# Performance work log

Hardware: AMD Instinct MI355X
Metric: run time of the kernel (lower is better)

Reference implementation:

```python
import jax, jax.numpy as jnp
import numpy as np

N = 100000   # nodes
E = 1600000  # edges
NF = 8       # node features
H = 128      # hid_channel


def _gcn(x, ei, W, b):
    """PyG GCNConv: add self-loops, sym-normalize, x@W then scatter-add, +bias."""
    n = x.shape[0]
    loop = jnp.arange(n)
    s = jnp.concatenate([ei[0], loop])
    d = jnp.concatenate([ei[1], loop])
    deg = jax.ops.segment_sum(jnp.ones_like(s, jnp.float32), d, num_segments=n)
    dinv = jnp.where(deg > 0, jax.lax.rsqrt(deg), 0.0)
    norm = dinv[s] * dinv[d]                       # [E+n]
    xw = x @ W                                     # [n, out]
    out = jax.ops.segment_sum(xw[s] * norm[:, None], d, num_segments=n)
    return out + b


def _dag_pool(x, ei, k):
    """DAGPool(k): contiguous-k mean clustering; unpool restores saved (x, ei)."""
    n = x.shape[0]
    nc = -(-n // k)
    cid = jnp.arange(n) // k
    cnt = jax.ops.segment_sum(jnp.ones((n,), jnp.float32), cid, num_segments=nc)
    xp = jax.ops.segment_sum(x, cid, num_segments=nc) / cnt[:, None]
    return xp, ei // k, (x, ei)


def setup_inputs() -> dict:
    key = jax.random.key(0)
    ks = jax.random.split(key, 24)

    def w(k, i, o):
        return jax.random.normal(k, (i, o), jnp.float32) / np.sqrt(i).astype(np.float32)

    d = {
        "x": jax.random.normal(ks[0], (N, NF), jnp.float32),
        "edge_index": jax.random.randint(ks[1], (E, 2), 0, N, dtype=jnp.int64),
        "c1W": w(ks[2], NF, H),          "c1b": jnp.zeros((H,), jnp.float32),
        "c2W": w(ks[3], H + NF, H),      "c2b": jnp.zeros((H,), jnp.float32),
        "c3W": w(ks[4], H + NF, H),      "c3b": jnp.zeros((H,), jnp.float32),
        "c4W": w(ks[5], H, H),           "c4b": jnp.zeros((H,), jnp.float32),
        "c5W": w(ks[6], H, H),           "c5b": jnp.zeros((H,), jnp.float32),
        "f1W": w(ks[7], 2 * H + NF, H),  "f1b": jnp.zeros((H,), jnp.float32),
        "f2W": w(ks[8], 2 * H, H),       "f2b": jnp.zeros((H,), jnp.float32),
        "f3W": w(ks[9], 2 * H, H),       "f3b": jnp.zeros((H,), jnp.float32),
        "f4W": w(ks[10], H + NF, H),     "f4b": jnp.zeros((H,), jnp.float32),
        "f5W": w(ks[11], H + NF, 1),     "f5b": jnp.zeros((1,), jnp.float32),
    }
    return d


def reference(x, edge_index, c1W, c1b, c2W, c2b, c3W, c3b, c4W, c4b, c5W, c5b,
              f1W, f1b, f2W, f2b, f3W, f3b, f4W, f4b, f5W, f5b):
    ei = edge_index.T  # [2, E]
    x_in = x
    h = jax.nn.relu(_gcn(x, ei, c1W, c1b))
    h = jnp.concatenate([h, x_in], axis=-1)
    h = jax.nn.relu(_gcn(h, ei, c2W, c2b))
    h = jnp.concatenate([x_in, h], axis=-1)            # [N, NF+H]

    xp1, ei1, un1 = _dag_pool(h, ei, 5)
    t = jax.nn.relu(_gcn(xp1, ei1, c3W, c3b))
    t = jax.nn.relu(jnp.concatenate([xp1, t], -1) @ f1W + f1b)
    xp2, ei2, un2 = _dag_pool(t, ei1, 3)
    t = jax.nn.relu(_gcn(xp2, ei2, c4W, c4b))
    t = jax.nn.relu(jnp.concatenate([xp2, t], -1) @ f2W + f2b)
    xp3, ei3, un3 = _dag_pool(t, ei2, 3)
    t = jax.nn.relu(_gcn(xp3, ei3, c5W, c5b))
    t = jax.nn.relu(jnp.concatenate([xp3, t], -1) @ f3W + f3b)
    # unpool chain discards pooled features and restores pre-pool1 state
    xr, _ = un1

    h = jax.nn.relu(xr @ f4W + f4b)
    out = jax.nn.sigmoid(jnp.concatenate([x_in, h], -1) @ f5W + f5b)
    return out.ravel()  # [N], binary (num_classes==2 -> 1 logit)
```

## Files before the change

kernel.cpp:

```cpp
#include <hip/hip_runtime.h>
#include <hip/hip_bf16.h>
#include <math.h>


#define NBUK 256

typedef __attribute__((ext_vector_type(8))) short short8;
typedef __attribute__((ext_vector_type(4))) float f32x4;

__device__ __forceinline__ unsigned short f32_to_bf16_rne(float f) {
    unsigned u = __float_as_uint(f);
    return (unsigned short)((u + 0x7fffu + ((u >> 16) & 1u)) >> 16);
}

__global__ __launch_bounds__(512) void bucket_kernel(
    const int* __restrict__ ei, int* __restrict__ bcnt_pad,
    int2* __restrict__ bucket, int E, int N, int cap) {
    constexpr int EPB = 4096;
    __shared__ int lcnt[NBUK];
    __shared__ int lcur[NBUK];
    int e0 = blockIdx.x * EPB;
    int e1 = min(e0 + EPB, E);
    if (threadIdx.x < NBUK) lcnt[threadIdx.x] = 0;
    __syncthreads();
    for (int e = e0 + threadIdx.x; e < e1; e += 512) {
        int2 v = ((const int2*)ei)[e];
        if ((unsigned)v.y < (unsigned)N) {
            int b = (int)(((unsigned long long)(unsigned)v.y * NBUK) / (unsigned)N);
            atomicAdd(&lcnt[b], 1);
        }
    }
    __syncthreads();
    if (threadIdx.x < NBUK)
        lcur[threadIdx.x] = atomicAdd(&bcnt_pad[threadIdx.x * 16], lcnt[threadIdx.x]);
    __syncthreads();
    for (int e = e0 + threadIdx.x; e < e1; e += 512) {
        int2 v = ((const int2*)ei)[e];
        if ((unsigned)v.y < (unsigned)N) {
            int b = (int)(((unsigned long long)(unsigned)v.y * NBUK) / (unsigned)N);
            int pos = atomicAdd(&lcur[b], 1);
            if (pos < cap) {
                int s = ((unsigned)v.x < (unsigned)N) ? v.x : 0;
                bucket[(size_t)b * cap + pos] = make_int2(s, v.y);
            }
        }
    }
}

__global__ __launch_bounds__(1024) void csr_kernel(
    const int2* __restrict__ bucket, const int* __restrict__ bcnt_pad,
    const float* __restrict__ x,
    int* __restrict__ cnt, int* __restrict__ rowstart, int* __restrict__ col,
    float* __restrict__ dinv, float* __restrict__ xs,
    unsigned short* __restrict__ Abf2, int N, int cap) {
    __shared__ int lcnt[1024];
    __shared__ int lscan[1024];
    int b = blockIdx.x;
    int lo = (int)(((long long)b * N + NBUK - 1) / NBUK);
    int hi = (int)(((long long)(b + 1) * N + NBUK - 1) / NBUK);
    int range = hi - lo;
    lcnt[threadIdx.x] = 0;
    __syncthreads();
    int n = min(bcnt_pad[b * 16], cap);
    const int2* bk = bucket + (size_t)b * cap;
    for (int i = threadIdx.x; i < n; i += 1024)
        atomicAdd(&lcnt[bk[i].y - lo], 1);
    __syncthreads();
    int myc = lcnt[threadIdx.x];
    if ((int)threadIdx.x < range) cnt[lo + threadIdx.x] = myc;
    lscan[threadIdx.x] = myc;
    __syncthreads();
    for (int off = 1; off < 1024; off <<= 1) {
        int y = (threadIdx.x >= off) ? lscan[threadIdx.x - off] : 0;
        __syncthreads();
        lscan[threadIdx.x] += y;
        __syncthreads();
    }
    int colbase = b * cap;
    int excl = lscan[threadIdx.x] - myc;
    if ((int)threadIdx.x < range) rowstart[lo + threadIdx.x] = colbase + excl;
    lcnt[threadIdx.x] = excl;
    __syncthreads();
    for (int i = threadIdx.x; i < n; i += 1024) {
        int2 v = bk[i];
        int pos = atomicAdd(&lcnt[v.y - lo], 1);
        col[(size_t)colbase + pos] = v.x;
    }
    if ((int)threadIdx.x < range) {
        int v = lo + threadIdx.x;
        float dv = rsqrtf((float)(myc + 1));
        dinv[v] = dv;
        const float4* x4 = (const float4*)x;
        float4 a = x4[v * 2], c = x4[v * 2 + 1];
        float4* o = (float4*)xs;
        o[v * 2]     = make_float4(a.x * dv, a.y * dv, a.z * dv, a.w * dv);
        o[v * 2 + 1] = make_float4(c.x * dv, c.y * dv, c.z * dv, c.w * dv);
        unsigned short u[8] = {f32_to_bf16_rne(a.x), f32_to_bf16_rne(a.y),
                               f32_to_bf16_rne(a.z), f32_to_bf16_rne(a.w),
                               f32_to_bf16_rne(c.x), f32_to_bf16_rne(c.y),
                               f32_to_bf16_rne(c.z), f32_to_bf16_rne(c.w)};
        ulonglong2 pk;
        pk.x = (unsigned long long)u[0] | ((unsigned long long)u[1] << 16)
             | ((unsigned long long)u[2] << 32) | ((unsigned long long)u[3] << 48);
        pk.y = (unsigned long long)u[4] | ((unsigned long long)u[5] << 16)
             | ((unsigned long long)u[6] << 32) | ((unsigned long long)u[7] << 48);
        *(ulonglong2*)&Abf2[(size_t)v * 160] = pk;
        ulonglong2 z; z.x = 0ull; z.y = 0ull;
        *(ulonglong2*)&Abf2[(size_t)v * 160 + 136] = z;
        *(ulonglong2*)&Abf2[(size_t)v * 160 + 144] = z;
        *(ulonglong2*)&Abf2[(size_t)v * 160 + 152] = z;
    }
}

__global__ __launch_bounds__(256) void agg8_kernel(const float* __restrict__ xs,
                                                   const int* __restrict__ rowstart,
                                                   const int* __restrict__ cnt,
                                                   const int* __restrict__ col,
                                                   const float* __restrict__ dinv,
                                                   float* __restrict__ aggx,
                                                   unsigned short* __restrict__ Abf,
                                                   int n) {
    int v = blockIdx.x * 256 + threadIdx.x;
    if (v >= n) return;
    const float4* r4 = (const float4*)xs;
    float4 a = make_float4(0, 0, 0, 0), b = make_float4(0, 0, 0, 0);
    int start = rowstart[v];
    int end = start + cnt[v];
    for (int j = start; j < end; j++) {
        int s = col[j];
        float4 p = r4[(size_t)s * 2], q = r4[(size_t)s * 2 + 1];
        a.x += p.x; a.y += p.y; a.z += p.z; a.w += p.w;
        b.x += q.x; b.y += q.y; b.z += q.z; b.w += q.w;
    }
    float4 p = r4[(size_t)v * 2], q = r4[(size_t)v * 2 + 1];
    a.x += p.x; a.y += p.y; a.z += p.z; a.w += p.w;
    b.x += q.x; b.y += q.y; b.z += q.z; b.w += q.w;
    float dv = dinv[v];
    a = make_float4(a.x * dv, a.y * dv, a.z * dv, a.w * dv);
    b = make_float4(b.x * dv, b.y * dv, b.z * dv, b.w * dv);
    float4* o = (float4*)aggx;
    o[(size_t)v * 2]     = a;
    o[(size_t)v * 2 + 1] = b;
    unsigned short u[8] = {f32_to_bf16_rne(a.x), f32_to_bf16_rne(a.y),
                           f32_to_bf16_rne(a.z), f32_to_bf16_rne(a.w),
                           f32_to_bf16_rne(b.x), f32_to_bf16_rne(b.y),
                           f32_to_bf16_rne(b.z), f32_to_bf16_rne(b.w)};
    ulonglong2 pk;
    pk.x = (unsigned long long)u[0] | ((unsigned long long)u[1] << 16)
         | ((unsigned long long)u[2] << 32) | ((unsigned long long)u[3] << 48);
    pk.y = (unsigned long long)u[4] | ((unsigned long long)u[5] << 16)
         | ((unsigned long long)u[6] << 32) | ((unsigned long long)u[7] << 48);
    *(ulonglong2*)&Abf[(size_t)v * 160 + 128] = pk;
    ulonglong2 z; z.x = 0ull; z.y = 0ull;
    *(ulonglong2*)&Abf[(size_t)v * 160 + 136] = z;
    *(ulonglong2*)&Abf[(size_t)v * 160 + 144] = z;
    *(ulonglong2*)&Abf[(size_t)v * 160 + 152] = z;
}

__global__ __launch_bounds__(256) void agg128_kernel(const unsigned* __restrict__ rows,
                                                     const int* __restrict__ rowstart,
                                                     const int* __restrict__ cnt,
                                                     const int* __restrict__ col,
                                                     const float* __restrict__ dinv,
                                                     unsigned short* __restrict__ Abf,
                                                     int n) {
    int v = blockIdx.x * 4 + (threadIdx.x >> 6);
    int lane = threadIdx.x & 63;
    if (v >= n) return;
    float ax = 0.f, ay = 0.f;
    int start = rowstart[v];
    int end = start + cnt[v];
    for (int base = start; base < end; base += 64) {
        int m = end - base; if (m > 64) m = 64;
        int si = (lane < m) ? col[base + lane] : 0;
        int t = 0;
        for (; t + 4 <= m; t += 4) {
            int s0 = __shfl(si, t),     s1 = __shfl(si, t + 1);
            int s2 = __shfl(si, t + 2), s3 = __shfl(si, t + 3);
            unsigned u0 = rows[(size_t)s0 * 64 + lane];
            unsigned u1 = rows[(size_t)s1 * 64 + lane];
            unsigned u2 = rows[(size_t)s2 * 64 + lane];
            unsigned u3 = rows[(size_t)s3 * 64 + lane];
            ax += (__uint_as_float(u0 << 16) + __uint_as_float(u1 << 16))
                + (__uint_as_float(u2 << 16) + __uint_as_float(u3 << 16));
            ay += (__uint_as_float(u0 & 0xffff0000u) + __uint_as_float(u1 & 0xffff0000u))
                + (__uint_as_float(u2 & 0xffff0000u) + __uint_as_float(u3 & 0xffff0000u));
        }
        for (; t < m; t++) {
            int s = __shfl(si, t);
            unsigned u = rows[(size_t)s * 64 + lane];
            ax += __uint_as_float(u << 16);
            ay += __uint_as_float(u & 0xffff0000u);
        }
    }
    unsigned us = rows[(size_t)v * 64 + lane];
    ax += __uint_as_float(us << 16);
    ay += __uint_as_float(us & 0xffff0000u);
    float dv = dinv[v];
    unsigned pk = (unsigned)f32_to_bf16_rne(ax * dv)
                | ((unsigned)f32_to_bf16_rne(ay * dv) << 16);
    ((unsigned*)Abf)[(size_t)v * 80 + lane] = pk;
}

__global__ __launch_bounds__(256) void gemm8_kernel(
    const float* __restrict__ A1, const float* __restrict__ W,
    const float* __restrict__ bias, const float* __restrict__ dinv,
    unsigned short* __restrict__ out, int n) {
    constexpr int K = 8, KP = 12, NPB = 32;
    __shared__ float lds[NPB * KP];
    int node0 = blockIdx.x * NPB;
    for (int idx = threadIdx.x; idx < NPB * K; idx += 256) {
        int r = idx / K, k = idx - r * K;
        int node = node0 + r;
        lds[r * KP + k] = (node < n) ? A1[(size_t)node * K + k] : 0.f;
    }
    __syncthreads();
    int f8 = threadIdx.x & 15, ng = threadIdx.x >> 4;
    int fbase = f8 * 8;
    float acc[2][8];
#pragma unroll
    for (int r = 0; r < 2; r++)
#pragma unroll
        for (int j = 0; j < 8; j++) acc[r][j] = 0.f;
    for (int k = 0; k < K; k += 4) {
        float4 wlo[4], whi[4];
#pragma unroll
        for (int kk = 0; kk < 4; kk++) {
            wlo[kk] = *(const float4*)&W[(size_t)(k + kk) * 128 + fbase];
            whi[kk] = *(const float4*)&W[(size_t)(k + kk) * 128 + fbase + 4];
        }
#pragma unroll
        for (int r = 0; r < 2; r++) {
            float4 a = *(const float4*)&lds[(2 * ng + r) * KP + k];
            float av[4] = {a.x, a.y, a.z, a.w};
#pragma unroll
            for (int kk = 0; kk < 4; kk++) {
                acc[r][0] += av[kk] * wlo[kk].x; acc[r][1] += av[kk] * wlo[kk].y;
                acc[r][2] += av[kk] * wlo[kk].z; acc[r][3] += av[kk] * wlo[kk].w;
                acc[r][4] += av[kk] * whi[kk].x; acc[r][5] += av[kk] * whi[kk].y;
                acc[r][6] += av[kk] * whi[kk].z; acc[r][7] += av[kk] * whi[kk].w;
            }
        }
    }
    float4 blo = *(const float4*)&bias[fbase];
    float4 bhi = *(const float4*)&bias[fbase + 4];
    float bv[8] = {blo.x, blo.y, blo.z, blo.w, bhi.x, bhi.y, bhi.z, bhi.w};
#pragma unroll
    for (int r = 0; r < 2; r++) {
        int node = node0 + 2 * ng + r;
        if (node < n) {
            float dv = dinv[node];
            unsigned short u[8];
#pragma unroll
            for (int j = 0; j < 8; j++)
                u[j] = f32_to_bf16_rne(fmaxf(acc[r][j] + bv[j], 0.f) * dv);
            ulonglong2 pk;
            pk.x = (unsigned long long)u[0] | ((unsigned long long)u[1] << 16)
                 | ((unsigned long long)u[2] << 32) | ((unsigned long long)u[3] << 48);
            pk.y = (unsigned long long)u[4] | ((unsigned long long)u[5] << 16)
                 | ((unsigned long long)u[6] << 32) | ((unsigned long long)u[7] << 48);
            *(ulonglong2*)&out[(size_t)node * 128 + fbase] = pk;
        }
    }
}

__global__ __launch_bounds__(256) void pack_w_kernel(const float* __restrict__ W,
                                                     unsigned short* __restrict__ wp, int K) {
    int t = blockIdx.x * 256 + threadIdx.x;
    if (t >= 20480) return;
    int i = t & 7, l = (t >> 3) & 63, fc = (t >> 9) & 7, ks = t >> 12;
    int k = ks * 32 + (l >> 4) * 8 + i;
    int c = (l & 15) + 16 * fc;
    float v = (k < K) ? W[(size_t)k * 128 + c] : 0.f;
    wp[t] = f32_to_bf16_rne(v);
}

template <int MODE>
__global__ __launch_bounds__(256) void mfma_gemm(
    const unsigned short* __restrict__ A, const unsigned short* __restrict__ wp,
    const float* __restrict__ bias, const float* __restrict__ x,
    const float* __restrict__ f5W, const float* __restrict__ f5b,
    void* __restrict__ outv, int n) {
    __shared__ float ldsx[64];
    int node0 = blockIdx.x * 64;
    if constexpr (MODE == 2) {
        if (threadIdx.x < 64) {
            int rc = min(node0 + (int)threadIdx.x, n - 1);
            float s = 0.f;
#pragma unroll
            for (int k = 0; k < 8; k++) s += x[(size_t)rc * 8 + k] * f5W[k];
            ldsx[threadIdx.x] = s;
        }
        __syncthreads();
    }
    int wave = threadIdx.x >> 6, lane = threadIdx.x & 63;
    int g = lane >> 4, r = lane & 15;
    int row0 = node0 + wave * 16;
    int arow = min(row0 + r, n - 1);

    short8 a[5];
#pragma unroll
    for (int ks = 0; ks < 5; ks++)
        a[ks] = *(const short8*)&A[(size_t)arow * 160 + ks * 32 + g * 8];

    f32x4 acc[8] = {};
#pragma unroll
    for (int ks = 0; ks < 5; ks++) {
#pragma unroll
        for (int fc = 0; fc < 8; fc++) {
            short8 w = *(const short8*)&wp[(size_t)((ks * 8 + fc) * 64 + lane) * 8];
            acc[fc] = __builtin_amdgcn_mfma_f32_16x16x32_bf16(a[ks], w, acc[fc], 0, 0, 0);
        }
    }

    if constexpr (MODE == 1) {
        unsigned short* out = (unsigned short*)outv;
#pragma unroll
        for (int fc = 0; fc < 8; fc++) {
            int c = r + 16 * fc;
            float bc = bias[c];
#pragma unroll
            for (int v = 0; v < 4; v++) {
                int row = row0 + 4 * g + v;
                if (row < n)
                    out[(size_t)row * 160 + 8 + c] =
                        f32_to_bf16_rne(fmaxf(acc[fc][v] + bc, 0.f));
            }
        }
    } else {
        float plog[4] = {0.f, 0.f, 0.f, 0.f};
#pragma unroll
        for (int fc = 0; fc < 8; fc++) {
            int c = r + 16 * fc;
            float bc = bias[c];
            float w5 = f5W[8 + c];
#pragma unroll
            for (int v = 0; v < 4; v++)
                plog[v] += fmaxf(acc[fc][v] + bc, 0.f) * w5;
        }
#pragma unroll
        for (int m = 1; m < 16; m <<= 1) {
#pragma unroll
            for (int v = 0; v < 4; v++) plog[v] += __shfl_xor(plog[v], m);
        }
        if (r == 0) {
            float* out = (float*)outv;
            float fb = f5b[0];
#pragma unroll
            for (int v = 0; v < 4; v++) {
                int row = row0 + 4 * g + v;
                if (row < n)
                    out[row] = 1.f / (1.f + expf(-(plog[v] + ldsx[wave * 16 + 4 * g + v] + fb)));
            }
        }
    }
}

extern "C" void kernel_launch(void* const* d_in, const int* in_sizes, int n_in,
                              void* d_out, int out_size, void* d_ws, size_t ws_size,
                              hipStream_t stream) {
    const float* x   = (const float*)d_in[0];
    const int*   ei  = (const int*)d_in[1];
    const float* c1W = (const float*)d_in[2];
    const float* c1b = (const float*)d_in[3];
    const float* c2W = (const float*)d_in[4];
    const float* c2b = (const float*)d_in[5];
    const float* f4W = (const float*)d_in[18];
    const float* f4b = (const float*)d_in[19];
    const float* f5W = (const float*)d_in[20];
    const float* f5b = (const float*)d_in[21];
    float* out = (float*)d_out;

    int N = in_sizes[0] / 8;
    int E = in_sizes[1] / 2;

    char* p = (char*)d_ws;
    auto alloc = [&](size_t bytes) {
        char* q = p;
        p += (bytes + 255) & ~(size_t)255;
        return q;
    };
    const int cap = 8192;
    int*            cnt      = (int*)alloc((size_t)N * 4);
    int*            rowstart = (int*)alloc((size_t)N * 4);
    int*            bcnt_pad = (int*)alloc(NBUK * 16 * 4);
    float*          dinv     = (float*)alloc((size_t)N * 4);
    int*            col      = (int*)alloc((size_t)NBUK * cap * 4);
    float*          xs       = (float*)alloc((size_t)N * 8 * 4);
    float*          aggx     = (float*)alloc((size_t)N * 8 * 4);
    unsigned short* bufH1    = (unsigned short*)alloc((size_t)N * 128 * 2);
    unsigned short* Abf      = (unsigned short*)alloc((size_t)N * 160 * 2);
    unsigned short* Abf2     = (unsigned short*)alloc((size_t)N * 160 * 2);
    unsigned short* wp2      = (unsigned short*)alloc(20480 * 2);
    unsigned short* wp4      = (unsigned short*)alloc(20480 * 2);

    int2* bucket = (int2*)bufH1;

    (void)hipMemsetAsync(bcnt_pad, 0, NBUK * 16 * 4, stream);

    pack_w_kernel<<<80, 256, 0, stream>>>(c2W, wp2, 136);
    pack_w_kernel<<<80, 256, 0, stream>>>(f4W, wp4, 136);

    int gB = (E + 4095) / 4096;
    bucket_kernel<<<gB, 512, 0, stream>>>(ei, bcnt_pad, bucket, E, N, cap);

    csr_kernel<<<NBUK, 1024, 0, stream>>>(bucket, bcnt_pad, x, cnt, rowstart, col,
                                          dinv, xs, Abf2, N, cap);

    int gN = (N + 255) / 256;
    agg8_kernel<<<gN, 256, 0, stream>>>(xs, rowstart, cnt, col, dinv, aggx, Abf, N);

    gemm8_kernel<<<(N + 31) / 32, 256, 0, stream>>>(aggx, c1W, c1b, dinv, bufH1, N);

    agg128_kernel<<<(N + 3) / 4, 256, 0, stream>>>((const unsigned*)bufH1, rowstart,
                                                   cnt, col, dinv, Abf, N);

    int g64 = (N + 63) / 64;
    mfma_gemm<1><<<g64, 256, 0, stream>>>(Abf, wp2, c2b, nullptr, nullptr, nullptr,
                                          Abf2, N);
    mfma_gemm<2><<<g64, 256, 0, stream>>>(Abf2, wp4, f4b, x, f5W, f5b, out, N);
}
```

Before: 199.6 us.

## Pack bucket entries, parallelize agg8 per feature, unroll agg128, merge weight packing

Bucket entries shrink from an int2 to a single 32-bit word holding the local destination offset in the high bits and the source index in the low 17 bits. This halves the bucket write and read traffic. agg8 now gives each node eight lanes, one per feature, and shares column indices through shuffles instead of running one thread per node over the whole edge list, which should improve load balance and coalescing. agg128 gains an 8-way unrolled gather loop for more memory-level parallelism, and the two weight-pack launches are merged into one. The 17-bit source field assumes N below 131072 and the local offset must fit in 15 bits.

```diff
diff --git a/kernel.cpp b/kernel.cpp
--- a/kernel.cpp
+++ b/kernel.cpp
@@ -15,7 +15,7 @@
 
 __global__ __launch_bounds__(512) void bucket_kernel(
     const int* __restrict__ ei, int* __restrict__ bcnt_pad,
-    int2* __restrict__ bucket, int E, int N, int cap) {
+    unsigned* __restrict__ bucket, int E, int N, int cap) {
     constexpr int EPB = 4096;
     __shared__ int lcnt[NBUK];
     __shared__ int lcur[NBUK];
@@ -40,15 +40,16 @@
             int b = (int)(((unsigned long long)(unsigned)v.y * NBUK) / (unsigned)N);
             int pos = atomicAdd(&lcur[b], 1);
             if (pos < cap) {
-                int s = ((unsigned)v.x < (unsigned)N) ? v.x : 0;
-                bucket[(size_t)b * cap + pos] = make_int2(s, v.y);
+                unsigned s = ((unsigned)v.x < (unsigned)N) ? (unsigned)v.x : 0u;
+                int lo = (b * N + NBUK - 1) >> 8;
+                bucket[(size_t)b * cap + pos] = ((unsigned)(v.y - lo) << 17) | s;
             }
         }
     }
 }
 
 __global__ __launch_bounds__(1024) void csr_kernel(
-    const int2* __restrict__ bucket, const int* __restrict__ bcnt_pad,
+    const unsigned* __restrict__ bucket, const int* __restrict__ bcnt_pad,
     const float* __restrict__ x,
     int* __restrict__ cnt, int* __restrict__ rowstart, int* __restrict__ col,
     float* __restrict__ dinv, float* __restrict__ xs,
@@ -62,9 +63,9 @@
     lcnt[threadIdx.x] = 0;
     __syncthreads();
     int n = min(bcnt_pad[b * 16], cap);
-    const int2* bk = bucket + (size_t)b * cap;
+    const unsigned* bk = bucket + (size_t)b * cap;
     for (int i = threadIdx.x; i < n; i += 1024)
-        atomicAdd(&lcnt[bk[i].y - lo], 1);
+        atomicAdd(&lcnt[bk[i] >> 17], 1);
     __syncthreads();
     int myc = lcnt[threadIdx.x];
     if ((int)threadIdx.x < range) cnt[lo + threadIdx.x] = myc;
@@ -82,9 +83,9 @@
     lcnt[threadIdx.x] = excl;
     __syncthreads();
     for (int i = threadIdx.x; i < n; i += 1024) {
-        int2 v = bk[i];
-        int pos = atomicAdd(&lcnt[v.y - lo], 1);
-        col[(size_t)colbase + pos] = v.x;
+        unsigned u = bk[i];
+        int pos = atomicAdd(&lcnt[u >> 17], 1);
+        col[(size_t)colbase + pos] = (int)(u & 0x1FFFFu);
     }
     if ((int)threadIdx.x < range) {
         int v = lo + threadIdx.x;
@@ -120,41 +121,31 @@
                                                    float* __restrict__ aggx,
                                                    unsigned short* __restrict__ Abf,
                                                    int n) {
-    int v = blockIdx.x * 256 + threadIdx.x;
+    int g = threadIdx.x >> 3;
+    int l = threadIdx.x & 7;
+    int v = blockIdx.x * 32 + g;
     if (v >= n) return;
-    const float4* r4 = (const float4*)xs;
-    float4 a = make_float4(0, 0, 0, 0), b = make_float4(0, 0, 0, 0);
     int start = rowstart[v];
-    int end = start + cnt[v];
-    for (int j = start; j < end; j++) {
-        int s = col[j];
-        float4 p = r4[(size_t)s * 2], q = r4[(size_t)s * 2 + 1];
-        a.x += p.x; a.y += p.y; a.z += p.z; a.w += p.w;
-        b.x += q.x; b.y += q.y; b.z += q.z; b.w += q.w;
-    }
-    float4 p = r4[(size_t)v * 2], q = r4[(size_t)v * 2 + 1];
-    a.x += p.x; a.y += p.y; a.z += p.z; a.w += p.w;
-    b.x += q.x; b.y += q.y; b.z += q.z; b.w += q.w;
+    int m = cnt[v];
+    float ax = 0.f;
+    for (int base = 0; base < m; base += 8) {
+        int mm = min(m - base, 8);
+        int si = (l < mm) ? col[start + base + l] : 0;
+#pragma unroll 8
+        for (int t = 0; t < 8; t++) {
+            if (t < mm) {
+                int s = __shfl(si, t, 8);
+                ax += xs[(size_t)s * 8 + l];
+            }
+        }
+    }
+    ax += xs[(size_t)v * 8 + l];
     float dv = dinv[v];
-    a = make_float4(a.x * dv, a.y * dv, a.z * dv, a.w * dv);
-    b = make_float4(b.x * dv, b.y * dv, b.z * dv, b.w * dv);
-    float4* o = (float4*)aggx;
-    o[(size_t)v * 2]     = a;
-    o[(size_t)v * 2 + 1] = b;
-    unsigned short u[8] = {f32_to_bf16_rne(a.x), f32_to_bf16_rne(a.y),
-                           f32_to_bf16_rne(a.z), f32_to_bf16_rne(a.w),
-                           f32_to_bf16_rne(b.x), f32_to_bf16_rne(b.y),
-                           f32_to_bf16_rne(b.z), f32_to_bf16_rne(b.w)};
-    ulonglong2 pk;
-    pk.x = (unsigned long long)u[0] | ((unsigned long long)u[1] << 16)
-         | ((unsigned long long)u[2] << 32) | ((unsigned long long)u[3] << 48);
-    pk.y = (unsigned long long)u[4] | ((unsigned long long)u[5] << 16)
-         | ((unsigned long long)u[6] << 32) | ((unsigned long long)u[7] << 48);
-    *(ulonglong2*)&Abf[(size_t)v * 160 + 128] = pk;
-    ulonglong2 z; z.x = 0ull; z.y = 0ull;
-    *(ulonglong2*)&Abf[(size_t)v * 160 + 136] = z;
-    *(ulonglong2*)&Abf[(size_t)v * 160 + 144] = z;
-    *(ulonglong2*)&Abf[(size_t)v * 160 + 152] = z;
+    ax *= dv;
+    aggx[(size_t)v * 8 + l] = ax;
+    Abf[(size_t)v * 160 + 128 + l] = f32_to_bf16_rne(ax);
+#pragma unroll 3
+    for (int t = l; t < 24; t += 8) Abf[(size_t)v * 160 + 136 + t] = 0;
 }
 
 __global__ __launch_bounds__(256) void agg128_kernel(const unsigned* __restrict__ rows,
@@ -174,6 +165,28 @@
         int m = end - base; if (m > 64) m = 64;
         int si = (lane < m) ? col[base + lane] : 0;
         int t = 0;
+        for (; t + 8 <= m; t += 8) {
+            int s0 = __shfl(si, t),     s1 = __shfl(si, t + 1);
+            int s2 = __shfl(si, t + 2), s3 = __shfl(si, t + 3);
+            int s4 = __shfl(si, t + 4), s5 = __shfl(si, t + 5);
+            int s6 = __shfl(si, t + 6), s7 = __shfl(si, t + 7);
+            unsigned u0 = rows[(size_t)s0 * 64 + lane];
+            unsigned u1 = rows[(size_t)s1 * 64 + lane];
+            unsigned u2 = rows[(size_t)s2 * 64 + lane];
+            unsigned u3 = rows[(size_t)s3 * 64 + lane];
+            unsigned u4 = rows[(size_t)s4 * 64 + lane];
+            unsigned u5 = rows[(size_t)s5 * 64 + lane];
+            unsigned u6 = rows[(size_t)s6 * 64 + lane];
+            unsigned u7 = rows[(size_t)s7 * 64 + lane];
+            ax += (__uint_as_float(u0 << 16) + __uint_as_float(u1 << 16))
+                + (__uint_as_float(u2 << 16) + __uint_as_float(u3 << 16))
+                + (__uint_as_float(u4 << 16) + __uint_as_float(u5 << 16))
+                + (__uint_as_float(u6 << 16) + __uint_as_float(u7 << 16));
+            ay += (__uint_as_float(u0 & 0xffff0000u) + __uint_as_float(u1 & 0xffff0000u))
+                + (__uint_as_float(u2 & 0xffff0000u) + __uint_as_float(u3 & 0xffff0000u))
+                + (__uint_as_float(u4 & 0xffff0000u) + __uint_as_float(u5 & 0xffff0000u))
+                + (__uint_as_float(u6 & 0xffff0000u) + __uint_as_float(u7 & 0xffff0000u));
+        }
         for (; t + 4 <= m; t += 4) {
             int s0 = __shfl(si, t),     s1 = __shfl(si, t + 1);
             int s2 = __shfl(si, t + 2), s3 = __shfl(si, t + 3);
@@ -264,14 +277,19 @@
     }
 }
 
-__global__ __launch_bounds__(256) void pack_w_kernel(const float* __restrict__ W,
-                                                     unsigned short* __restrict__ wp, int K) {
-    int t = blockIdx.x * 256 + threadIdx.x;
+__global__ __launch_bounds__(256) void pack_w_kernel(const float* __restrict__ W1,
+                                                     const float* __restrict__ W2,
+                                                     unsigned short* __restrict__ wp1,
+                                                     unsigned short* __restrict__ wp2) {
+    int tt = blockIdx.x * 256 + threadIdx.x;
+    const float* W = (tt < 20480) ? W1 : W2;
+    unsigned short* wp = (tt < 20480) ? wp1 : wp2;
+    int t = (tt < 20480) ? tt : tt - 20480;
     if (t >= 20480) return;
     int i = t & 7, l = (t >> 3) & 63, fc = (t >> 9) & 7, ks = t >> 12;
     int k = ks * 32 + (l >> 4) * 8 + i;
     int c = (l & 15) + 16 * fc;
-    float v = (k < K) ? W[(size_t)k * 128 + c] : 0.f;
+    float v = (k < 136) ? W[(size_t)k * 128 + c] : 0.f;
     wp[t] = f32_to_bf16_rne(v);
 }
 
@@ -394,12 +412,11 @@
     unsigned short* wp2      = (unsigned short*)alloc(20480 * 2);
     unsigned short* wp4      = (unsigned short*)alloc(20480 * 2);
 
-    int2* bucket = (int2*)bufH1;
+    unsigned* bucket = (unsigned*)bufH1;
 
     (void)hipMemsetAsync(bcnt_pad, 0, NBUK * 16 * 4, stream);
 
-    pack_w_kernel<<<80, 256, 0, stream>>>(c2W, wp2, 136);
-    pack_w_kernel<<<80, 256, 0, stream>>>(f4W, wp4, 136);
+    pack_w_kernel<<<160, 256, 0, stream>>>(c2W, f4W, wp2, wp4);
 
     int gB = (E + 4095) / 4096;
     bucket_kernel<<<gB, 512, 0, stream>>>(ei, bcnt_pad, bucket, E, N, cap);
@@ -407,8 +424,8 @@
     csr_kernel<<<NBUK, 1024, 0, stream>>>(bucket, bcnt_pad, x, cnt, rowstart, col,
                                           dinv, xs, Abf2, N, cap);
 
-    int gN = (N + 255) / 256;
-    agg8_kernel<<<gN, 256, 0, stream>>>(xs, rowstart, cnt, col, dinv, aggx, Abf, N);
+    agg8_kernel<<<(N + 31) / 32, 256, 0, stream>>>(xs, rowstart, cnt, col, dinv,
+                                                   aggx, Abf, N);
 
     gemm8_kernel<<<(N + 31) / 32, 256, 0, stream>>>(aggx, c1W, c1b, dinv, bufH1, N);
 
```

After: 189.6 us, median of 2. 5.0% less time.
